# Kernel optimization log

Measured on AMD Instinct MI355X. Metric: run time of the kernel, lower is better.

## Reference

```python
import jax, jax.numpy as jnp
import numpy as np

EPS = 1e-12  # torch F.normalize eps


def _l2_normalize(x, axis=-1):
    n = jnp.linalg.norm(x, axis=axis, keepdims=True)
    return x / jnp.maximum(n, EPS)


def setup_inputs() -> dict:
    key = jax.random.key(0)
    k1, k2 = jax.random.split(key)
    B, N, D, V = 4, 512, 768, 50257
    return {
        "query": jax.random.normal(k1, (B, N, D), dtype=jnp.float32),
        "key_embeddings": jax.random.normal(k2, (V, D), dtype=jnp.float32),
        "alpha_raw": jnp.float32(0.5),  # learnable scalar parameter (init_alpha)
        "k": 64,
    }


def reference(query, key_embeddings, alpha_raw, k):
    # query: [B,N,D], key_embeddings: [V,D]
    query_norm = _l2_normalize(query)            # [B,N,D]
    key_norm = _l2_normalize(key_embeddings)     # [V,D]
    # node-level cosine similarity, max-pooled over nodes
    node_sim = jnp.einsum('bnd,vd->bnv', query_norm, key_norm)  # [B,N,V]
    node_sim_pool = node_sim.max(axis=1)                        # [B,V]
    # graph-level similarity from mean of normalized node features
    graph_query = query_norm.mean(axis=1)                       # [B,D]
    graph_sim = jnp.einsum('bd,vd->bv', graph_query, key_norm)  # [B,V]
    alpha = jax.nn.sigmoid(alpha_raw)
    fused_similarity = alpha * node_sim_pool + (1.0 - alpha) * graph_sim  # [B,V]
    _, topk_indices = jax.lax.top_k(fused_similarity, k)        # [B,k]
    selected_keys = key_embeddings[topk_indices]                # [B,k,D]
    return selected_keys, topk_indices, fused_similarity, alpha
```

## Files before the change

kernel.cpp:

```cpp
#include <hip/hip_runtime.h>
#include <hip/hip_bf16.h>
#include <math.h>

#define D 768
#define BQ 4
#define NQ 512
#define M_TOTAL (BQ*NQ)
#define KSEL 64

typedef short bf16x8 __attribute__((ext_vector_type(8)));
typedef float f32x4  __attribute__((ext_vector_type(4)));

__device__ __forceinline__ void split1(float x, unsigned int& h, unsigned int& l)
{
    unsigned int u  = __float_as_uint(x);
    unsigned int hb = (u + 0x7fffu + ((u >> 16) & 1u)) & 0xffff0000u;
    h = hb >> 16;
    l = __float_as_uint(x - __uint_as_float(hb)) >> 16;
}


__global__ __launch_bounds__(768)
void split_invnorm_kernel(const float* __restrict__ x, unsigned short* __restrict__ sp,
                          float* __restrict__ inv, int rows_src, int rows_dst)
{
    __shared__ float red[768];
    const int tid  = threadIdx.x;
    const int rloc = tid / 96;
    const int c    = (tid % 96) * 8;
    const int row  = blockIdx.x * 8 + rloc;
    if (row >= rows_dst) return;
    const int src  = row < rows_src ? row : rows_src - 1;

    const float* rp = x + (size_t)src * D + c;
    float4 a = *reinterpret_cast<const float4*>(rp);
    float4 b = *reinterpret_cast<const float4*>(rp + 4);

    unsigned int h0,h1,h2,h3,h4,h5,h6,h7, l0,l1,l2,l3,l4,l5,l6,l7;
    split1(a.x,h0,l0); split1(a.y,h1,l1); split1(a.z,h2,l2); split1(a.w,h3,l3);
    split1(b.x,h4,l4); split1(b.y,h5,l5); split1(b.z,h6,l6); split1(b.w,h7,l7);
    uint4 hv, lv;
    hv.x = h0 | (h1<<16); hv.y = h2 | (h3<<16); hv.z = h4 | (h5<<16); hv.w = h6 | (h7<<16);
    lv.x = l0 | (l1<<16); lv.y = l2 | (l3<<16); lv.z = l4 | (l5<<16); lv.w = l6 | (l7<<16);

    unsigned short* dh = sp + (size_t)row * (2*D) + c;
    *reinterpret_cast<uint4*>(dh)     = hv;
    *reinterpret_cast<uint4*>(dh + D) = lv;

    float ss = a.x*a.x + a.y*a.y + a.z*a.z + a.w*a.w
             + b.x*b.x + b.y*b.y + b.z*b.z + b.w*b.w;
    red[tid] = ss;
    __syncthreads();
    if ((tid % 96) == 0 && row < rows_src) {
        float s = 0.f;
        #pragma unroll
        for (int j = 0; j < 96; ++j) s += red[rloc*96 + j];
        inv[row] = 1.0f / fmaxf(sqrtf(s), 1e-12f);
    }
}

#define GBM 256
#define GBN 256
#define GBK 32
#define GNT (D/GBK)
#define SLOT_B_OFF 32768
#define SLOT_SZ 65536

__device__ __forceinline__ void gload16(const unsigned short* g, char* l)
{
    __builtin_amdgcn_global_load_lds((const __attribute__((address_space(1))) void*)g,
                                     (__attribute__((address_space(3))) void*)l, 16, 0, 0);
}

__global__ __launch_bounds__(512, 2)
void fast_gemm(const unsigned short* __restrict__ Qsp, const unsigned short* __restrict__ Ksp,
               const float* __restrict__ invq, float* __restrict__ pmax, float* __restrict__ psum,
               int Vp, int gx)
{
    extern __shared__ char smem[];

    const int t    = threadIdx.x;
    const int lane = t & 63;
    const int w    = t >> 6;
    const int wr   = w >> 2;
    const int wc   = w & 3;

    int lid = blockIdx.x;
    int u   = (lid & 7) * gx + (lid >> 3);
    const int by = u & 7;
    const int bx = u >> 3;
    const int m0 = by * GBM;
    const int v0 = bx * GBN;

    const int lrow = lane >> 3;
    const int cc   = (lane & 7) ^ lrow;
    const size_t goff = (size_t)lrow * (2*D) + (size_t)(cc >> 2) * D + (size_t)(cc & 3) * 8;

    const int rAbase = ((w & 3) << 3) + ((w >> 2) << 7);
    const int rBbase = w * 32;

    const unsigned short* gAsrc = Qsp + (size_t)(m0 + rAbase) * (2*D) + goff;
    const unsigned short* gBsrc = Ksp + (size_t)(v0 + rBbase) * (2*D) + goff;

    #define SAk(k_, sl_, j_) gload16(gAsrc + (k_) + (size_t)(j_)*32*(2*D), (sl_) + (rAbase + (j_)*32)*128)
    #define SBk(k_, sl_, j_) gload16(gBsrc + (k_) + (size_t)(j_)*8 *(2*D), (sl_) + SLOT_B_OFF + (rBbase + (j_)*8)*128)

    const int l15 = lane & 15, kg = lane >> 4;
    const int sHi = ((kg    ) ^ (lane & 7)) * 16;
    const int sLo = ((kg + 4) ^ (lane & 7)) * 16;
    const int offA = (wr*128 + l15) * 128;
    const int offB = SLOT_B_OFF + (wc*64 + l15) * 128;

    f32x4 acc[8][4];
    #pragma unroll
    for (int i = 0; i < 8; ++i)
        #pragma unroll
        for (int j = 0; j < 4; ++j)
            acc[i][j] = f32x4{0.f,0.f,0.f,0.f};

    bf16x8 Bh[4], Bl[4];

    char* sl0 = smem;
    char* sl1 = smem + SLOT_SZ;

    SBk(0, sl0, 0); SBk(0, sl0, 1); SAk(0, sl0, 0);
    SBk(0, sl0, 2); SBk(0, sl0, 3); SAk(0, sl0, 1);
    SAk(0, sl0, 2); SAk(0, sl0, 3);
    asm volatile("s_waitcnt vmcnt(2)" ::: "memory");
    __builtin_amdgcn_s_barrier();

    #define PHASE(p_, STG, VMW) do {                                                         \
        bf16x8 Ah0 = *(const bf16x8*)(scur + offA + (2*(p_)  )*2048 + sHi);                  \
        bf16x8 Al0 = *(const bf16x8*)(scur + offA + (2*(p_)  )*2048 + sLo);                  \
        bf16x8 Ah1 = *(const bf16x8*)(scur + offA + (2*(p_)+1)*2048 + sHi);                  \
        bf16x8 Al1 = *(const bf16x8*)(scur + offA + (2*(p_)+1)*2048 + sLo);                  \
        STG;                                                                                 \
        __builtin_amdgcn_s_barrier();                                                        \
        asm volatile("s_waitcnt lgkmcnt(0)" ::: "memory");                                   \
        __builtin_amdgcn_s_setprio(1);                                                       \
        _Pragma("unroll")                                                                    \
        for (int nf = 0; nf < 4; ++nf) {                                                     \
            acc[2*(p_)  ][nf] = __builtin_amdgcn_mfma_f32_16x16x32_bf16(Ah0, Bh[nf], acc[2*(p_)  ][nf], 0,0,0); \
            acc[2*(p_)+1][nf] = __builtin_amdgcn_mfma_f32_16x16x32_bf16(Ah1, Bh[nf], acc[2*(p_)+1][nf], 0,0,0); \
        }                                                                                    \
        _Pragma("unroll")                                                                    \
        for (int nf = 0; nf < 4; ++nf) {                                                     \
            acc[2*(p_)  ][nf] = __builtin_amdgcn_mfma_f32_16x16x32_bf16(Ah0, Bl[nf], acc[2*(p_)  ][nf], 0,0,0); \
            acc[2*(p_)+1][nf] = __builtin_amdgcn_mfma_f32_16x16x32_bf16(Ah1, Bl[nf], acc[2*(p_)+1][nf], 0,0,0); \
        }                                                                                    \
        _Pragma("unroll")                                                                    \
        for (int nf = 0; nf < 4; ++nf) {                                                     \
            acc[2*(p_)  ][nf] = __builtin_amdgcn_mfma_f32_16x16x32_bf16(Al0, Bh[nf], acc[2*(p_)  ][nf], 0,0,0); \
            acc[2*(p_)+1][nf] = __builtin_amdgcn_mfma_f32_16x16x32_bf16(Al1, Bh[nf], acc[2*(p_)+1][nf], 0,0,0); \
        }                                                                                    \
        __builtin_amdgcn_s_setprio(0);                                                       \
        VMW;                                                                                 \
        __builtin_amdgcn_s_barrier();                                                        \
    } while(0)

    for (int T = 0; T < GNT; ++T) {
        const bool st = (T + 1 < GNT);
        char* scur = (T & 1) ? sl1 : sl0;
        char* snxt = (T & 1) ? sl0 : sl1;
        const int k1 = (T + 1) * GBK;

        #pragma unroll
        for (int nf = 0; nf < 4; ++nf) {
            Bh[nf] = *(const bf16x8*)(scur + offB + nf*2048 + sHi);
            Bl[nf] = *(const bf16x8*)(scur + offB + nf*2048 + sLo);
        }
        PHASE(0, { if (st) { SBk(k1, snxt, 0); SBk(k1, snxt, 1); SAk(k1, snxt, 0); } }, );
        PHASE(1, { if (st) { SBk(k1, snxt, 2); SBk(k1, snxt, 3); SAk(k1, snxt, 1); } },
                 { if (st) asm volatile("s_waitcnt vmcnt(6)" ::: "memory");
                   else    asm volatile("s_waitcnt vmcnt(0)" ::: "memory"); });
        PHASE(2, { if (st) SAk(k1, snxt, 2); }, );
        PHASE(3, { if (st) SAk(k1, snxt, 3); },
                 { if (st) asm volatile("s_waitcnt vmcnt(2)" ::: "memory"); });
    }
    #undef PHASE
    #undef SAk
    #undef SBk

    __syncthreads();
    float iq[32];
    #pragma unroll
    for (int mf = 0; mf < 8; ++mf)
        #pragma unroll
        for (int r = 0; r < 4; ++r)
            iq[mf*4+r] = invq[m0 + wr*128 + mf*16 + kg*4 + r];

    float* redm = (float*)smem;
    float* reds = redm + 512;
    #pragma unroll
    for (int nf = 0; nf < 4; ++nf) {
        float pmv = -INFINITY, psv = 0.f;
        #pragma unroll
        for (int mf = 0; mf < 8; ++mf)
            #pragma unroll
            for (int r = 0; r < 4; ++r) {
                float x = acc[mf][nf][r] * iq[mf*4+r];
                pmv = fmaxf(pmv, x);
                psv += x;
            }
        pmv = fmaxf(pmv, __shfl_xor(pmv, 16, 64));
        pmv = fmaxf(pmv, __shfl_xor(pmv, 32, 64));
        psv += __shfl_xor(psv, 16, 64);
        psv += __shfl_xor(psv, 32, 64);
        if (lane < 16) {
            redm[wr*256 + wc*64 + nf*16 + l15] = pmv;
            reds[wr*256 + wc*64 + nf*16 + l15] = psv;
        }
    }
    __syncthreads();
    if (t < 256) {
        pmax[(size_t)by * Vp + v0 + t] = fmaxf(redm[t], redm[256+t]);
        psum[(size_t)by * Vp + v0 + t] = reds[t] + reds[256+t];
    }
}

__global__ void blend_kernel(const float* __restrict__ pmax, const float* __restrict__ psum,
                             const float* __restrict__ invk, const float* __restrict__ alpha_raw,
                             float* __restrict__ out_fused, float* __restrict__ out_alpha,
                             int V, int Vp)
{
    int v = blockIdx.x * 256 + threadIdx.x;
    float alpha = 1.0f / (1.0f + expf(-alpha_raw[0]));
    if (blockIdx.x == 0 && threadIdx.x == 0) out_alpha[0] = alpha;
    if (v >= V) return;
    float ik = invk[v];
    #pragma unroll
    for (int b = 0; b < BQ; ++b) {
        float nm = fmaxf(pmax[(size_t)(2*b)*Vp + v], pmax[(size_t)(2*b+1)*Vp + v]) * ik;
        float gs = (psum[(size_t)(2*b)*Vp + v] + psum[(size_t)(2*b+1)*Vp + v]) * ik * (1.0f/(float)NQ);
        out_fused[(size_t)b*V + v] = alpha*nm + (1.0f-alpha)*gs;
    }
}

__device__ __forceinline__ unsigned int mono_map(float f)
{
    unsigned int u = __float_as_uint(f);
    return u ^ ((u & 0x80000000u) ? 0xFFFFFFFFu : 0x80000000u);
}

__global__ __launch_bounds__(1024)
void topk_radix_kernel(const float* __restrict__ fused,
                       int* __restrict__ idxout, float* __restrict__ out_idx, int V)
{
    const int b = blockIdx.x, t = threadIdx.x;
    const float* row = fused + (size_t)b * V;

    __shared__ unsigned int hist[256];
    __shared__ unsigned int sh_pref;
    __shared__ int sh_kneed;
    __shared__ unsigned int sh_nA, sh_nE;
    __shared__ unsigned long long key[64];
    __shared__ int eqIdx[256];

    unsigned int pref = 0;
    int kneed = KSEL;
    #pragma unroll
    for (int p = 24; p >= 0; p -= 8) {
        if (t < 256) hist[t] = 0;
        __syncthreads();
        unsigned int mask = (p == 24) ? 0u : (0xFFFFFFFFu << (p + 8));
        for (int i = t; i < V; i += 1024) {
            unsigned int u = mono_map(row[i]);
            if ((u & mask) == pref)
                atomicAdd(&hist[(u >> p) & 255u], 1u);
        }
        __syncthreads();
        if (t == 0) {
            int cum = 0, sel = 0;
            for (int bb = 255; bb >= 0; --bb) {
                int c = (int)hist[bb];
                if (cum + c >= kneed) { sel = bb; break; }
                cum += c;
            }
            sh_pref  = pref | ((unsigned int)sel << p);
            sh_kneed = kneed - cum;
        }
        __syncthreads();
        pref  = sh_pref;
        kneed = sh_kneed;
        __syncthreads();
    }

    const unsigned int T = pref;
    if (t == 0) { sh_nA = 0; sh_nE = 0; }
    __syncthreads();
    for (int i = t; i < V; i += 1024) {
        unsigned int u = mono_map(row[i]);
        if (u > T) {
            unsigned int pos = atomicAdd(&sh_nA, 1u);
            if (pos < 64) key[pos] = ((unsigned long long)(~u) << 32) | (unsigned int)i;
        } else if (u == T) {
            unsigned int pos = atomicAdd(&sh_nE, 1u);
            if (pos < 256) eqIdx[pos] = i;
        }
    }
    __syncthreads();
    const int nA = (int)sh_nA;
    const int nE = (int)sh_nE;
    if (t < 256 && t >= min(nE, 256)) eqIdx[t] = 0x7fffffff;
    __syncthreads();
    if (nE > 1) {
        for (int k = 2; k <= 256; k <<= 1)
            for (int j = k >> 1; j > 0; j >>= 1) {
                if (t < 256) {
                    int ixj = t ^ j;
                    if (ixj > t) {
                        int a = eqIdx[t], c = eqIdx[ixj];
                        bool up = ((t & k) == 0);
                        if ((a > c) == up) { eqIdx[t] = c; eqIdx[ixj] = a; }
                    }
                }
                __syncthreads();
            }
    }
    if (t < kneed)
        key[nA + t] = ((unsigned long long)(~T) << 32) | (unsigned int)eqIdx[t];
    __syncthreads();
    for (int k = 2; k <= 64; k <<= 1)
        for (int j = k >> 1; j > 0; j >>= 1) {
            if (t < 64) {
                int ixj = t ^ j;
                if (ixj > t) {
                    unsigned long long a = key[t], c = key[ixj];
                    bool up = ((t & k) == 0);
                    if ((a > c) == up) { key[t] = c; key[ixj] = a; }
                }
            }
            __syncthreads();
        }
    if (t < KSEL) {
        int idx = (int)(unsigned int)(key[t] & 0xFFFFFFFFull);
        idxout[b*KSEL + t]  = idx;
        out_idx[b*KSEL + t] = (float)idx;
    }
}

__global__ void gather_kernel(const int* __restrict__ idx, const float* __restrict__ Kmat,
                              float* __restrict__ out_sel)
{
    int j = blockIdx.x & 63, b = blockIdx.x >> 6, t = threadIdx.x;
    int sel = idx[b*KSEL + j];
    float4 v = *reinterpret_cast<const float4*>(Kmat + (size_t)sel * D + t*4);
    *reinterpret_cast<float4*>(out_sel + ((size_t)(b*KSEL + j)) * D + t*4) = v;
}

#define BMT 128
#define BVT 128
#define NSTEP (D/32)

__global__ void row_invnorm_kernel(const float* __restrict__ x, float* __restrict__ inv, int rows)
{
    int wid  = (blockIdx.x * blockDim.x + threadIdx.x) >> 6;
    int lane = threadIdx.x & 63;
    if (wid >= rows) return;
    const float* r = x + (size_t)wid * D;
    float ss = 0.f;
    #pragma unroll
    for (int s = 0; s < 3; ++s) {
        float4 v = *reinterpret_cast<const float4*>(r + s*256 + lane*4);
        ss += v.x*v.x + v.y*v.y + v.z*v.z + v.w*v.w;
    }
    #pragma unroll
    for (int off = 32; off > 0; off >>= 1)
        ss += __shfl_xor(ss, off, 64);
    if (lane == 0) inv[wid] = 1.0f / fmaxf(sqrtf(ss), 1e-12f);
}

__global__ void compute_gq_kernel(const float* __restrict__ q, const float* __restrict__ invq,
                                  float* __restrict__ gq)
{
    int t = blockIdx.x * blockDim.x + threadIdx.x;
    if (t >= BQ*D) return;
    int b = t / D, d = t - b*D;
    float acc = 0.f;
    const float* qb = q + (size_t)b * NQ * D + d;
    const float* iq = invq + b*NQ;
    for (int n = 0; n < NQ; ++n)
        acc += iq[n] * qb[(size_t)n*D];
    gq[t] = acc * (1.0f/(float)NQ);
}

__device__ __forceinline__ void split8(float4 a, float4 b, uint4& hi, uint4& lo)
{
    unsigned int h0,h1,h2,h3,h4,h5,h6,h7, l0,l1,l2,l3,l4,l5,l6,l7;
    split1(a.x,h0,l0); split1(a.y,h1,l1); split1(a.z,h2,l2); split1(a.w,h3,l3);
    split1(b.x,h4,l4); split1(b.y,h5,l5); split1(b.z,h6,l6); split1(b.w,h7,l7);
    hi.x = h0 | (h1<<16); hi.y = h2 | (h3<<16); hi.z = h4 | (h5<<16); hi.w = h6 | (h7<<16);
    lo.x = l0 | (l1<<16); lo.y = l2 | (l3<<16); lo.z = l4 | (l5<<16); lo.w = l6 | (l7<<16);
}

__global__ __launch_bounds__(256)
void mfma_gemm_maxpool(const float* __restrict__ Q, const float* __restrict__ Kmat,
                       const float* __restrict__ invq, const float* __restrict__ invk,
                       float* __restrict__ partial, int V, int Vp)
{
    __shared__ __align__(16) unsigned short lds[16384];
    const int t    = threadIdx.x;
    const int lane = t & 63;
    const int w    = t >> 6;
    const int wr   = w >> 1;
    const int wc   = w & 1;
    const int v0   = blockIdx.x * BVT;
    const int m0   = blockIdx.y * BMT;

    const int srow = t >> 1;
    const int scol = (t & 1) * 16;
    const int c0   = (t & 1) * 2;
    const unsigned int ps0 = (c0     + (srow >> 1)) & 3;
    const unsigned int ps1 = (c0 + 1 + (srow >> 1)) & 3;
    const unsigned int wO0 = srow*32 + ps0*8;
    const unsigned int wO1 = srow*32 + ps1*8;

    const float* Ap = Q + (size_t)(m0 + srow) * D + scol;
    int vrow = v0 + srow; if (vrow > V-1) vrow = V-1;
    const float* Bp = Kmat + (size_t)vrow * D + scol;

    const int lr = lane & 15, kg = lane >> 4;
    const int arowb = wr*64 + lr;
    const int browb = wc*64 + lr;
    const unsigned int slotA = (kg + (arowb >> 1)) & 3;
    const unsigned int slotB = (kg + (browb >> 1)) & 3;
    const unsigned int offA = arowb*32 + slotA*8;
    const unsigned int offB = browb*32 + slotB*8;

    f32x4 acc[4][4];
    #pragma unroll
    for (int i = 0; i < 4; ++i)
        #pragma unroll
        for (int j = 0; j < 4; ++j)
            acc[i][j] = f32x4{0.f,0.f,0.f,0.f};

    float4 ra0,ra1,ra2,ra3, rb0,rb1,rb2,rb3;
    #define LOADSTEP(s_) do { \
        const float* ap_ = Ap + (s_)*32; const float* bp_ = Bp + (s_)*32; \
        ra0 = *(const float4*)(ap_);    ra1 = *(const float4*)(ap_+4); \
        ra2 = *(const float4*)(ap_+8);  ra3 = *(const float4*)(ap_+12); \
        rb0 = *(const float4*)(bp_);    rb1 = *(const float4*)(bp_+4); \
        rb2 = *(const float4*)(bp_+8);  rb3 = *(const float4*)(bp_+12); \
    } while(0)

    LOADSTEP(0);
    for (int s = 0; s < NSTEP; ++s) {
        uint4 ah0,al0, ah1,al1, bh0,bl0, bh1,bl1;
        split8(ra0,ra1, ah0,al0); split8(ra2,ra3, ah1,al1);
        split8(rb0,rb1, bh0,bl0); split8(rb2,rb3, bh1,bl1);
        __syncthreads();
        *(uint4*)&lds[        wO0] = ah0;  *(uint4*)&lds[ 4096 + wO0] = al0;
        *(uint4*)&lds[        wO1] = ah1;  *(uint4*)&lds[ 4096 + wO1] = al1;
        *(uint4*)&lds[ 8192 + wO0] = bh0;  *(uint4*)&lds[12288 + wO0] = bl0;
        *(uint4*)&lds[ 8192 + wO1] = bh1;  *(uint4*)&lds[12288 + wO1] = bl1;
        if (s + 1 < NSTEP) LOADSTEP(s + 1);
        __syncthreads();

        bf16x8 Ah[4], Al[4], Bh[4], Bl[4];
        #pragma unroll
        for (int fm = 0; fm < 4; ++fm) {
            unsigned int o = offA + fm*512;
            Ah[fm] = *(const bf16x8*)&lds[o];
            Al[fm] = *(const bf16x8*)&lds[4096 + o];
        }
        #pragma unroll
        for (int fv = 0; fv < 4; ++fv) {
            unsigned int o = offB + fv*512;
            Bh[fv] = *(const bf16x8*)&lds[8192 + o];
            Bl[fv] = *(const bf16x8*)&lds[12288 + o];
        }
        #pragma unroll
        for (int fm = 0; fm < 4; ++fm)
            #pragma unroll
            for (int fv = 0; fv < 4; ++fv) {
                acc[fm][fv] = __builtin_amdgcn_mfma_f32_16x16x32_bf16(Ah[fm], Bh[fv], acc[fm][fv], 0,0,0);
                acc[fm][fv] = __builtin_amdgcn_mfma_f32_16x16x32_bf16(Ah[fm], Bl[fv], acc[fm][fv], 0,0,0);
                acc[fm][fv] = __builtin_amdgcn_mfma_f32_16x16x32_bf16(Al[fm], Bh[fv], acc[fm][fv], 0,0,0);
            }
    }
    #undef LOADSTEP

    __syncthreads();
    float* red = (float*)lds;
    float iq[4][4];
    #pragma unroll
    for (int fm = 0; fm < 4; ++fm)
        #pragma unroll
        for (int r = 0; r < 4; ++r)
            iq[fm][r] = invq[m0 + wr*64 + fm*16 + kg*4 + r];
    #pragma unroll
    for (int fv = 0; fv < 4; ++fv) {
        float tm = -INFINITY;
        #pragma unroll
        for (int fm = 0; fm < 4; ++fm)
            #pragma unroll
            for (int r = 0; r < 4; ++r)
                tm = fmaxf(tm, acc[fm][fv][r] * iq[fm][r]);
        tm = fmaxf(tm, __shfl_xor(tm, 16, 64));
        tm = fmaxf(tm, __shfl_xor(tm, 32, 64));
        if (lane < 16) red[wr*128 + wc*64 + fv*16 + lane] = tm;
    }
    __syncthreads();
    if (t < 128) {
        int v = v0 + t;
        if (v < V)
            partial[(size_t)blockIdx.y * Vp + v] = fmaxf(red[t], red[128 + t]) * invk[v];
    }
}

__global__ void fused_sim_kernel(const float* __restrict__ Kmat, const float* __restrict__ invk,
                                 const float* __restrict__ gq, const float* __restrict__ partial,
                                 const float* __restrict__ alpha_raw,
                                 float* __restrict__ out_fused, float* __restrict__ out_alpha,
                                 int V, int Vp)
{
    int wib  = threadIdx.x >> 6;
    int lane = threadIdx.x & 63;
    float alpha = 1.0f / (1.0f + expf(-alpha_raw[0]));
    if (blockIdx.x == 0 && threadIdx.x == 0) out_alpha[0] = alpha;
    int v = blockIdx.x * 4 + wib;
    if (v >= V) return;
    const float* kr = Kmat + (size_t)v * D;
    float accb[BQ] = {0.f,0.f,0.f,0.f};
    #pragma unroll
    for (int s = 0; s < 3; ++s) {
        float4 kv = *reinterpret_cast<const float4*>(kr + s*256 + lane*4);
        #pragma unroll
        for (int b = 0; b < BQ; ++b) {
            float4 gv = *reinterpret_cast<const float4*>(gq + b*D + s*256 + lane*4);
            accb[b] += gv.x*kv.x + gv.y*kv.y + gv.z*kv.z + gv.w*kv.w;
        }
    }
    #pragma unroll
    for (int b = 0; b < BQ; ++b)
        #pragma unroll
        for (int off = 32; off > 0; off >>= 1)
            accb[b] += __shfl_xor(accb[b], off, 64);
    if (lane < BQ) {
        int b = lane;
        float node = partial[(size_t)(b*4+0)*Vp + v];
        #pragma unroll
        for (int i = 1; i < 4; ++i)
            node = fmaxf(node, partial[(size_t)(b*4+i)*Vp + v]);
        float graph = accb[b] * invk[v];
        out_fused[(size_t)b*V + v] = alpha*node + (1.0f-alpha)*graph;
    }
}

__global__ __launch_bounds__(1024)
void topk_gather_kernel(const float* __restrict__ fused, const float* __restrict__ Kmat,
                        float* __restrict__ scratch, float* __restrict__ out_sel,
                        float* __restrict__ out_idx, int V, int Vp)
{
    const int b = blockIdx.x, t = threadIdx.x;
    const int lane = t & 63, wid = t >> 6;
    const float* row = fused + (size_t)b * V;
    float* s = scratch + (size_t)b * Vp;
    for (int i = t; i < V; i += 1024) s[i] = row[i];
    __syncthreads();

    const int CH = (V + 1023) / 1024;
    const int lo = t * CH;
    const int hi = min(V, lo + CH);
    float lmax = -INFINITY; int lidx = 0x7fffffff;
    for (int i = lo; i < hi; ++i) { float x = s[i]; if (x > lmax) { lmax = x; lidx = i; } }

    __shared__ float swv[16];
    __shared__ int   swi[16];
    __shared__ int   sbest;

    for (int j = 0; j < KSEL; ++j) {
        float v = lmax; int id = lidx;
        #pragma unroll
        for (int off = 32; off > 0; off >>= 1) {
            float ov = __shfl_xor(v, off, 64);
            int   oi = __shfl_xor(id, off, 64);
            if (ov > v || (ov == v && oi < id)) { v = ov; id = oi; }
        }
        if (lane == 0) { swv[wid] = v; swi[wid] = id; }
        __syncthreads();
        if (t == 0) {
            float bv = swv[0]; int bi = swi[0];
            for (int x = 1; x < 16; ++x)
                if (swv[x] > bv || (swv[x] == bv && swi[x] < bi)) { bv = swv[x]; bi = swi[x]; }
            sbest = bi;
            out_idx[b*KSEL + j] = (float)bi;
        }
        __syncthreads();
        const int sel = sbest;
        if (sel >= lo && sel < hi) {
            s[sel] = -INFINITY;
            lmax = -INFINITY; lidx = 0x7fffffff;
            for (int i = lo; i < hi; ++i) { float x = s[i]; if (x > lmax) { lmax = x; lidx = i; } }
        }
        if (t < 192) {
            float4 kv = *reinterpret_cast<const float4*>(&Kmat[(size_t)sel * D + t*4]);
            *reinterpret_cast<float4*>(&out_sel[((size_t)b*KSEL + j)*D + t*4]) = kv;
        }
        __syncthreads();
    }
}

extern "C" void kernel_launch(void* const* d_in, const int* in_sizes, int n_in,
                              void* d_out, int out_size, void* d_ws, size_t ws_size,
                              hipStream_t stream)
{
    const float* q         = (const float*)d_in[0];
    const float* kemb      = (const float*)d_in[1];
    const float* alpha_raw = (const float*)d_in[2];
    int V = in_sizes[1] / D;

    float* out_sel   = (float*)d_out;
    float* out_idx   = out_sel + BQ*KSEL*D;
    float* out_fused = out_idx + BQ*KSEL;
    float* out_alpha = out_fused + (size_t)BQ*V;

    size_t Vp = (size_t)((V + 255) & ~255);
    float* ws      = (float*)d_ws;
    float* invk    = ws;
    float* invq    = invk + Vp;
    float* pmax    = invq + M_TOTAL;
    float* psum    = pmax + 8*Vp;
    float* scratch = psum + 8*Vp;
    int*   idxbuf  = (int*)(scratch + 4*Vp);
    unsigned short* Qsp = (unsigned short*)(idxbuf + 256);
    unsigned short* Ksp = Qsp + (size_t)M_TOTAL * (2*D);
    size_t need = (size_t)((char*)(Ksp + Vp*(2*D)) - (char*)d_ws);

    if (ws_size >= need) {
        split_invnorm_kernel<<<M_TOTAL/8, 768, 0, stream>>>(q, Qsp, invq, M_TOTAL, M_TOTAL);
        split_invnorm_kernel<<<(int)(Vp/8), 768, 0, stream>>>(kemb, Ksp, invk, V, (int)Vp);

        hipFuncSetAttribute(reinterpret_cast<const void*>(fast_gemm),
                            hipFuncAttributeMaxDynamicSharedMemorySize, 2*SLOT_SZ);

        int gx = (int)(Vp / GBN);
        fast_gemm<<<gx*8, 512, 2*SLOT_SZ, stream>>>(Qsp, Ksp, invq, pmax, psum, (int)Vp, gx);

        blend_kernel<<<(V + 255)/256, 256, 0, stream>>>(pmax, psum, invk, alpha_raw,
                                                        out_fused, out_alpha, V, (int)Vp);
        topk_radix_kernel<<<BQ, 1024, 0, stream>>>(out_fused, idxbuf, out_idx, V);
        gather_kernel<<<BQ*KSEL, 192, 0, stream>>>(idxbuf, kemb, out_sel);
    } else {
        int Vp2 = (V + 127) & ~127;
        float* f_invk    = ws;
        float* f_invq    = f_invk + Vp2;
        float* f_gq      = f_invq + M_TOTAL;
        float* f_partial = f_gq + BQ*D;
        float* f_scratch = f_partial + (size_t)16*Vp2;

        row_invnorm_kernel<<<(V + 3)/4, 256, 0, stream>>>(kemb, f_invk, V);
        row_invnorm_kernel<<<(M_TOTAL + 3)/4, 256, 0, stream>>>(q, f_invq, M_TOTAL);
        compute_gq_kernel<<<(BQ*D + 255)/256, 256, 0, stream>>>(q, f_invq, f_gq);

        dim3 g(Vp2 / BVT, M_TOTAL / BMT);
        mfma_gemm_maxpool<<<g, 256, 0, stream>>>(q, kemb, f_invq, f_invk, f_partial, V, Vp2);

        fused_sim_kernel<<<(V + 3)/4, 256, 0, stream>>>(kemb, f_invk, f_gq, f_partial, alpha_raw,
                                                        out_fused, out_alpha, V, Vp2);
        topk_gather_kernel<<<BQ, 1024, 0, stream>>>(out_fused, kemb, f_scratch, out_sel, out_idx, V, Vp2);
    }
}
```

Measured before the change: 523.4 us.

## Fuse blend, top-k and gather into one kernel; merge split launches

Merges the two split/inverse-norm launches for queries and keys into a single grid, and folds the blend, radix top-k and gather steps into one kernel with one block per batch. The fused similarity is recomputed from pmax/psum/invk on every radix pass instead of being read back from a materialized array, which removes launches and intermediate traffic. In exchange, only 4 blocks now do the blend work, and each pass reads 5 arrays rather than 1. The gather also runs on just those 4 blocks instead of 256.

```diff
diff --git a/kernel.cpp b/kernel.cpp
--- a/kernel.cpp
+++ b/kernel.cpp
@@ -21,16 +21,25 @@
 
 
 __global__ __launch_bounds__(768)
-void split_invnorm_kernel(const float* __restrict__ x, unsigned short* __restrict__ sp,
-                          float* __restrict__ inv, int rows_src, int rows_dst)
+void split_invnorm2_kernel(const float* __restrict__ q, const float* __restrict__ k,
+                           unsigned short* __restrict__ Qsp, unsigned short* __restrict__ Ksp,
+                           float* __restrict__ invq, float* __restrict__ invk,
+                           int qblocks, int V)
 {
     __shared__ float red[768];
     const int tid  = threadIdx.x;
     const int rloc = tid / 96;
     const int c    = (tid % 96) * 8;
-    const int row  = blockIdx.x * 8 + rloc;
-    if (row >= rows_dst) return;
-    const int src  = row < rows_src ? row : rows_src - 1;
+
+    const float* x; unsigned short* sp; float* inv; int rows_src, row;
+    if ((int)blockIdx.x < qblocks) {
+        x = q;  sp = Qsp; inv = invq; rows_src = M_TOTAL;
+        row = blockIdx.x * 8 + rloc;
+    } else {
+        x = k;  sp = Ksp; inv = invk; rows_src = V;
+        row = (blockIdx.x - qblocks) * 8 + rloc;
+    }
+    const int src = row < rows_src ? row : rows_src - 1;
 
     const float* rp = x + (size_t)src * D + c;
     float4 a = *reinterpret_cast<const float4*>(rp);
@@ -218,36 +227,35 @@
     }
 }
 
-__global__ void blend_kernel(const float* __restrict__ pmax, const float* __restrict__ psum,
-                             const float* __restrict__ invk, const float* __restrict__ alpha_raw,
-                             float* __restrict__ out_fused, float* __restrict__ out_alpha,
-                             int V, int Vp)
-{
-    int v = blockIdx.x * 256 + threadIdx.x;
-    float alpha = 1.0f / (1.0f + expf(-alpha_raw[0]));
-    if (blockIdx.x == 0 && threadIdx.x == 0) out_alpha[0] = alpha;
-    if (v >= V) return;
-    float ik = invk[v];
-    #pragma unroll
-    for (int b = 0; b < BQ; ++b) {
-        float nm = fmaxf(pmax[(size_t)(2*b)*Vp + v], pmax[(size_t)(2*b+1)*Vp + v]) * ik;
-        float gs = (psum[(size_t)(2*b)*Vp + v] + psum[(size_t)(2*b+1)*Vp + v]) * ik * (1.0f/(float)NQ);
-        out_fused[(size_t)b*V + v] = alpha*nm + (1.0f-alpha)*gs;
-    }
-}
-
 __device__ __forceinline__ unsigned int mono_map(float f)
 {
     unsigned int u = __float_as_uint(f);
     return u ^ ((u & 0x80000000u) ? 0xFFFFFFFFu : 0x80000000u);
 }
 
+__device__ __forceinline__ float blend_val(const float* __restrict__ pmax,
+                                           const float* __restrict__ psum,
+                                           const float* __restrict__ invk,
+                                           int b, int Vp, int i, float alpha)
+{
+    float ik = invk[i];
+    float nm = fmaxf(pmax[(size_t)(2*b)*Vp + i], pmax[(size_t)(2*b+1)*Vp + i]) * ik;
+    float gs = (psum[(size_t)(2*b)*Vp + i] + psum[(size_t)(2*b+1)*Vp + i]) * ik * (1.0f/(float)NQ);
+    return alpha*nm + (1.0f-alpha)*gs;
+}
+
 __global__ __launch_bounds__(1024)
-void topk_radix_kernel(const float* __restrict__ fused,
-                       int* __restrict__ idxout, float* __restrict__ out_idx, int V)
+void blend_topk_gather_kernel(const float* __restrict__ pmax, const float* __restrict__ psum,
+                              const float* __restrict__ invk, const float* __restrict__ alpha_raw,
+                              const float* __restrict__ Kmat,
+                              float* __restrict__ out_fused, float* __restrict__ out_alpha,
+                              float* __restrict__ out_idx, float* __restrict__ out_sel,
+                              int V, int Vp)
 {
     const int b = blockIdx.x, t = threadIdx.x;
-    const float* row = fused + (size_t)b * V;
+    const float alpha = 1.0f / (1.0f + expf(-alpha_raw[0]));
+    if (b == 0 && t == 0) out_alpha[0] = alpha;
+    float* rowout = out_fused + (size_t)b * V;
 
     __shared__ unsigned int hist[256];
     __shared__ unsigned int sh_pref;
@@ -264,7 +272,9 @@
         __syncthreads();
         unsigned int mask = (p == 24) ? 0u : (0xFFFFFFFFu << (p + 8));
         for (int i = t; i < V; i += 1024) {
-            unsigned int u = mono_map(row[i]);
+            float f = blend_val(pmax, psum, invk, b, Vp, i, alpha);
+            if (p == 24) rowout[i] = f;
+            unsigned int u = mono_map(f);
             if ((u & mask) == pref)
                 atomicAdd(&hist[(u >> p) & 255u], 1u);
         }
@@ -289,7 +299,7 @@
     if (t == 0) { sh_nA = 0; sh_nE = 0; }
     __syncthreads();
     for (int i = t; i < V; i += 1024) {
-        unsigned int u = mono_map(row[i]);
+        unsigned int u = mono_map(blend_val(pmax, psum, invk, b, Vp, i, alpha));
         if (u > T) {
             unsigned int pos = atomicAdd(&sh_nA, 1u);
             if (pos < 64) key[pos] = ((unsigned long long)(~u) << 32) | (unsigned int)i;
@@ -332,20 +342,21 @@
             }
             __syncthreads();
         }
+    __syncthreads();
     if (t < KSEL) {
         int idx = (int)(unsigned int)(key[t] & 0xFFFFFFFFull);
-        idxout[b*KSEL + t]  = idx;
         out_idx[b*KSEL + t] = (float)idx;
     }
-}
-
-__global__ void gather_kernel(const int* __restrict__ idx, const float* __restrict__ Kmat,
-                              float* __restrict__ out_sel)
-{
-    int j = blockIdx.x & 63, b = blockIdx.x >> 6, t = threadIdx.x;
-    int sel = idx[b*KSEL + j];
-    float4 v = *reinterpret_cast<const float4*>(Kmat + (size_t)sel * D + t*4);
-    *reinterpret_cast<float4*>(out_sel + ((size_t)(b*KSEL + j)) * D + t*4) = v;
+    {
+        int j   = t >> 4;
+        int l16 = t & 15;
+        int sel = (int)(unsigned int)(key[j] & 0xFFFFFFFFull);
+        const float4* src = reinterpret_cast<const float4*>(Kmat + (size_t)sel * D);
+        float4* dst = reinterpret_cast<float4*>(out_sel + ((size_t)b*KSEL + j) * D);
+        #pragma unroll
+        for (int s = 0; s < 12; ++s)
+            dst[l16 + s*16] = src[l16 + s*16];
+    }
 }
 
 #define BMT 128
@@ -628,8 +639,10 @@
     size_t need = (size_t)((char*)(Ksp + Vp*(2*D)) - (char*)d_ws);
 
     if (ws_size >= need) {
-        split_invnorm_kernel<<<M_TOTAL/8, 768, 0, stream>>>(q, Qsp, invq, M_TOTAL, M_TOTAL);
-        split_invnorm_kernel<<<(int)(Vp/8), 768, 0, stream>>>(kemb, Ksp, invk, V, (int)Vp);
+        int qblocks = M_TOTAL / 8;
+        int kblocks = (int)(Vp / 8);
+        split_invnorm2_kernel<<<qblocks + kblocks, 768, 0, stream>>>(
+            q, kemb, Qsp, Ksp, invq, invk, qblocks, V);
 
         hipFuncSetAttribute(reinterpret_cast<const void*>(fast_gemm),
                             hipFuncAttributeMaxDynamicSharedMemorySize, 2*SLOT_SZ);
@@ -637,10 +650,9 @@
         int gx = (int)(Vp / GBN);
         fast_gemm<<<gx*8, 512, 2*SLOT_SZ, stream>>>(Qsp, Ksp, invq, pmax, psum, (int)Vp, gx);
 
-        blend_kernel<<<(V + 255)/256, 256, 0, stream>>>(pmax, psum, invk, alpha_raw,
-                                                        out_fused, out_alpha, V, (int)Vp);
-        topk_radix_kernel<<<BQ, 1024, 0, stream>>>(out_fused, idxbuf, out_idx, V);
-        gather_kernel<<<BQ*KSEL, 192, 0, stream>>>(idxbuf, kemb, out_sel);
+        blend_topk_gather_kernel<<<BQ, 1024, 0, stream>>>(
+            pmax, psum, invk, alpha_raw, kemb,
+            out_fused, out_alpha, out_idx, out_sel, V, (int)Vp);
     } else {
         int Vp2 = (V + 127) & ~127;
         float* f_invk    = ws;
```

Result: no change. 528.0 us (+0.9%).
